# Kernel optimization log

Measured on AMD Instinct MI355X. Metric: run time of the kernel, lower is better.

The kernel has to match this reference:

```python
import jax, jax.numpy as jnp
import numpy as np

N_NODES = 50000
N_EDGES = 1600000
D = 128        # fea_dim == hidden_units == dim_z
L = 3          # num_layers


def _gin_params(key, scale=0.05):
    ks = jax.random.split(key, 7)
    return dict(
        W1=jax.random.normal(ks[0], (L, D, D), jnp.float32) * scale,
        b1=jnp.zeros((L, D), jnp.float32),
        W2=jax.random.normal(ks[1], (L, D, D), jnp.float32) * scale,
        b2=jnp.zeros((L, D), jnp.float32),
        eps=jnp.zeros((L,), jnp.float32),
        Wout=jax.random.normal(ks[2], (D, D), jnp.float32) * scale,
        bout=jnp.zeros((D,), jnp.float32),
    )


def setup_inputs() -> dict:
    key = jax.random.key(0)
    k_x, k_s, k_d, k_m, k_sd = jax.random.split(key, 5)
    inp = {
        'x': jax.random.normal(k_x, (N_NODES, D), jnp.float32),
        'edge_src': jax.random.randint(k_s, (N_EDGES,), 0, N_NODES, jnp.int32),
        'edge_dst': jax.random.randint(k_d, (N_EDGES,), 0, N_NODES, jnp.int32),
    }
    for pref, k in (('mean_', k_m), ('std_', k_sd)):
        for name, v in _gin_params(k).items():
            inp[pref + name] = v
    inp['ln_gamma'] = jnp.ones((D,), jnp.float32)
    inp['ln_beta'] = jnp.zeros((D,), jnp.float32)
    return inp


def _gin(x, src, dst, W1, b1, W2, b2, eps, Wout, bout):
    # Standard GIN: h = MLP((1+eps)*h + sum_{j->i} h_j), Sigmoid activation
    h = x
    n = x.shape[0]
    for l in range(L):
        agg = jax.ops.segment_sum(h[src], dst, num_segments=n)  # [N, D]
        h = (1.0 + eps[l]) * h + agg
        h = jax.nn.sigmoid(h @ W1[l] + b1[l]) @ W2[l] + b2[l]
    return h @ Wout + bout  # [N, dim_z]


def _layernorm(v, g, b, eps=1e-5):
    m = jnp.mean(v, axis=-1, keepdims=True)
    var = jnp.var(v, axis=-1, keepdims=True)
    return (v - m) * jax.lax.rsqrt(var + eps) * g + b


def reference(x, edge_src, edge_dst,
              mean_W1, mean_b1, mean_W2, mean_b2, mean_eps, mean_Wout, mean_bout,
              std_W1, std_b1, std_W2, std_b2, std_eps, std_Wout, std_bout,
              ln_gamma, ln_beta):
    mean_v = _layernorm(_gin(x, edge_src, edge_dst, mean_W1, mean_b1, mean_W2,
                             mean_b2, mean_eps, mean_Wout, mean_bout),
                        ln_gamma, ln_beta)
    # NOTE: source applies bn_mean to the std path too (faithful to bug)
    std_v = _layernorm(_gin(x, edge_src, edge_dst, std_W1, std_b1, std_W2,
                            std_b2, std_eps, std_Wout, std_bout),
                       ln_gamma, ln_beta)
    epsilon = jax.random.normal(jax.random.key(42), mean_v.shape, mean_v.dtype)
    samples = mean_v + epsilon * std_v
    return (samples, mean_v, std_v)
```

## Files before the change

### kernel.cpp

```cpp
#include <hip/hip_runtime.h>
#include <math.h>

#define NNODES 50000
#define NEDGES 1600000
#define DIM    128
#define NHID   (NNODES * DIM)
#define TPB    256
#define NTILES ((NNODES + 63) / 64)

#define NBINS  196
#define BINSZ  256
#define EPT    16
#define CHUNK  (TPB * EPT)
#define NCHUNKS ((NEDGES + CHUNK - 1) / CHUNK)
#define BINCAP 10240

typedef unsigned short bf16_t;
typedef __attribute__((ext_vector_type(8))) short short8;
typedef __attribute__((ext_vector_type(4))) float f32x4;

__device__ __forceinline__ float bf_lo(unsigned u) { return __uint_as_float(u << 16); }
__device__ __forceinline__ float bf_hi(unsigned u) { return __uint_as_float(u & 0xFFFF0000u); }
__device__ __forceinline__ bf16_t f2bf(float f) {
    unsigned u = __float_as_uint(f);
    u += 0x7FFFu + ((u >> 16) & 1u);
    return (bf16_t)(u >> 16);
}
__device__ __forceinline__ unsigned pack2bf(float a, float b) {
    return (unsigned)f2bf(a) | ((unsigned)f2bf(b) << 16);
}

union S8U { short8 v; uint4 u4; unsigned us[4]; };

__global__ __launch_bounds__(TPB) void bin_hist_kernel(
    const int* __restrict__ dst, int* __restrict__ gcnt)
{
    __shared__ int lcnt[NBINS];
    const int tid = threadIdx.x;
    for (int i = tid; i < NBINS; i += TPB) lcnt[i] = 0;
    __syncthreads();
    const int base = blockIdx.x * CHUNK;
    #pragma unroll
    for (int k = 0; k < EPT; ++k) {
        int e = base + k * TPB + tid;
        if (e < NEDGES) atomicAdd(&lcnt[dst[e] >> 8], 1);
    }
    __syncthreads();
    for (int i = tid; i < NBINS; i += TPB) {
        int c = lcnt[i];
        if (c) atomicAdd(&gcnt[i], c);
    }
}

__global__ __launch_bounds__(64) void bin_scan_kernel(
    const int* __restrict__ gcnt, int* __restrict__ start, int* __restrict__ bcur,
    int* __restrict__ off)
{
    const int lane = threadIdx.x;
    int c[4];
    int s = 0;
    #pragma unroll
    for (int k = 0; k < 4; ++k) {
        int b = 4 * lane + k;
        c[k] = (b < NBINS) ? gcnt[b] : 0;
        s += c[k];
    }
    int incl = s;
    #pragma unroll
    for (int d = 1; d < 64; d <<= 1) {
        int t = __shfl_up(incl, d);
        if (lane >= d) incl += t;
    }
    int excl = incl - s;
    #pragma unroll
    for (int k = 0; k < 4; ++k) {
        int b = 4 * lane + k;
        if (b < NBINS) { start[b] = excl; bcur[b] = excl; }
        excl += c[k];
    }
    if (lane == 63) { start[NBINS] = excl; off[NNODES] = excl; }
}

__global__ __launch_bounds__(TPB) void bin_scatter_kernel(
    const int* __restrict__ src, const int* __restrict__ dst,
    int* __restrict__ bcur, unsigned* __restrict__ bucket)
{
    __shared__ int lcnt[NBINS];
    __shared__ int lcur[NBINS];
    const int tid = threadIdx.x;
    for (int i = tid; i < NBINS; i += TPB) lcnt[i] = 0;
    __syncthreads();

    unsigned pk[EPT];
    int bn[EPT];
    const int base = blockIdx.x * CHUNK;
    #pragma unroll
    for (int k = 0; k < EPT; ++k) {
        int e = base + k * TPB + tid;
        int b = -1; unsigned p = 0;
        if (e < NEDGES) {
            int d = dst[e];
            int s = src[e];
            b = d >> 8;
            p = ((unsigned)(d & 255) << 16) | (unsigned)s;
            atomicAdd(&lcnt[b], 1);
        }
        pk[k] = p; bn[k] = b;
    }
    __syncthreads();
    for (int i = tid; i < NBINS; i += TPB) {
        int c = lcnt[i];
        lcur[i] = (c > 0) ? atomicAdd(&bcur[i], c) : 0;
    }
    __syncthreads();
    #pragma unroll
    for (int k = 0; k < EPT; ++k) {
        if (bn[k] >= 0) {
            int p = atomicAdd(&lcur[bn[k]], 1);
            bucket[p] = pk[k];
        }
    }
}

__global__ __launch_bounds__(TPB) void build_csr_kernel(
    const int* __restrict__ start, unsigned* __restrict__ bucket,
    int* __restrict__ off)
{
    __shared__ unsigned se[BINCAP];
    __shared__ int lcnt[BINSZ];
    __shared__ int lofs[BINSZ];
    __shared__ int wsum[4];
    const int tid = threadIdx.x;
    const int b = blockIdx.x;
    const int j0 = start[b], j1 = start[b + 1];
    const int n = j1 - j0;

    lcnt[tid] = 0;
    for (int i = tid; i < n; i += TPB) se[i] = bucket[j0 + i];
    __syncthreads();
    for (int i = tid; i < n; i += TPB) atomicAdd(&lcnt[se[i] >> 16], 1);
    __syncthreads();

    const int lane = tid & 63, wid = tid >> 6;
    int v = lcnt[tid];
    int s = v;
    #pragma unroll
    for (int d = 1; d < 64; d <<= 1) {
        int t = __shfl_up(s, d);
        if (lane >= d) s += t;
    }
    if (lane == 63) wsum[wid] = s;
    __syncthreads();
    if (tid == 0) {
        int a = 0;
        #pragma unroll
        for (int k = 0; k < 4; ++k) { int t = wsum[k]; wsum[k] = a; a += t; }
    }
    __syncthreads();
    int excl = wsum[wid] + s - v;
    lofs[tid] = excl;
    int node = b * BINSZ + tid;
    if (node < NNODES) off[node] = j0 + excl;
    __syncthreads();

    for (int i = tid; i < n; i += TPB) {
        unsigned e = se[i];
        int pos = atomicAdd(&lofs[e >> 16], 1);
        bucket[j0 + pos] = e & 0xFFFFu;
    }
}

__global__ __launch_bounds__(TPB) void gather_agg_f32_kernel(
    const float* __restrict__ h, const int* __restrict__ off,
    const unsigned* __restrict__ bucket, float* __restrict__ agg)
{
    int node = blockIdx.x * (TPB / 64) + (threadIdx.x >> 6);
    int lane = threadIdx.x & 63;
    if (node >= NNODES) return;
    int j0 = off[node], j1 = off[node + 1];
    const float* base = h + 2 * lane;
    float ax = 0.0f, ay = 0.0f;
    int j = j0;
    for (; j + 8 <= j1; j += 8) {
        unsigned s[8];
        #pragma unroll
        for (int k = 0; k < 8; ++k) s[k] = bucket[j + k];
        float2 v[8];
        #pragma unroll
        for (int k = 0; k < 8; ++k) v[k] = *(const float2*)(base + (size_t)s[k] * DIM);
        #pragma unroll
        for (int k = 0; k < 8; ++k) { ax += v[k].x; ay += v[k].y; }
    }
    for (; j < j1; ++j) {
        float2 v0 = *(const float2*)(base + (size_t)bucket[j] * DIM);
        ax += v0.x; ay += v0.y;
    }
    *(float2*)(agg + (size_t)node * DIM + 2 * lane) = make_float2(ax, ay);
}

__global__ __launch_bounds__(TPB) void gather_agg_bf16_kernel(
    const bf16_t* __restrict__ hb, const int* __restrict__ off,
    const unsigned* __restrict__ bucket, float* __restrict__ agg)
{
    int node = blockIdx.x * (TPB / 64) + (threadIdx.x >> 6);
    int lane = threadIdx.x & 63;
    if (node >= NNODES) return;
    int j0 = off[node], j1 = off[node + 1];
    const unsigned* base = (const unsigned*)hb + lane;
    float ax = 0.0f, ay = 0.0f;
    int j = j0;
    for (; j + 8 <= j1; j += 8) {
        unsigned s[8];
        #pragma unroll
        for (int k = 0; k < 8; ++k) s[k] = bucket[j + k];
        unsigned u[8];
        #pragma unroll
        for (int k = 0; k < 8; ++k) u[k] = base[(size_t)s[k] * (DIM / 2)];
        #pragma unroll
        for (int k = 0; k < 8; ++k) { ax += bf_lo(u[k]); ay += bf_hi(u[k]); }
    }
    for (; j < j1; ++j) {
        unsigned u0 = base[(size_t)bucket[j] * (DIM / 2)];
        ax += bf_lo(u0); ay += bf_hi(u0);
    }
    *(float2*)(agg + (size_t)node * DIM + 2 * lane) = make_float2(ax, ay);
}

template <class HinT>
__global__ __launch_bounds__(TPB, 2) void fused_layer_kernel(
    const HinT* __restrict__ hin, const float* __restrict__ agg,
    const float* __restrict__ eps_ptr, int eps_idx,
    const float* __restrict__ W1, const float* __restrict__ b1,
    const float* __restrict__ W2, const float* __restrict__ b2,
    bf16_t* __restrict__ out)
{
    __shared__ short sW1t[128 * 136];
    __shared__ short sW2t[128 * 136];
    float* y1buf = (float*)sW1t;

    const int tid = threadIdx.x;
    #pragma unroll
    for (int it = 0; it < 8; ++it) {
        int idx = it * 256 + tid;
        int n = idx & 127, koct = idx >> 7;
        float f1[8], f2[8];
        #pragma unroll
        for (int j = 0; j < 8; ++j) {
            f1[j] = W1[(8 * koct + j) * 128 + n];
            f2[j] = W2[(8 * koct + j) * 128 + n];
        }
        uint4 u1, u2;
        u1.x = pack2bf(f1[0], f1[1]); u1.y = pack2bf(f1[2], f1[3]);
        u1.z = pack2bf(f1[4], f1[5]); u1.w = pack2bf(f1[6], f1[7]);
        u2.x = pack2bf(f2[0], f2[1]); u2.y = pack2bf(f2[2], f2[3]);
        u2.z = pack2bf(f2[4], f2[5]); u2.w = pack2bf(f2[6], f2[7]);
        *(uint4*)&sW1t[n * 136 + 8 * koct] = u1;
        *(uint4*)&sW2t[n * 136 + 8 * koct] = u2;
    }
    __syncthreads();

    const int lane = tid & 63, w = tid >> 6;
    const int m = lane & 15, quad = lane >> 4;

    short8 bf1[32];
    #pragma unroll
    for (int c = 0; c < 8; ++c)
        #pragma unroll
        for (int k0 = 0; k0 < 4; ++k0)
            bf1[c * 4 + k0] = *(const short8*)&sW1t[(16 * c + m) * 136 + 32 * k0 + 8 * quad];
    __syncthreads();

    const float scale = 1.0f + eps_ptr[eps_idx];
    float b1v[8], b2v[8];
    #pragma unroll
    for (int c = 0; c < 8; ++c) { b1v[c] = b1[16 * c + m]; b2v[c] = b2[16 * c + m]; }

    const int t = blockIdx.x;
    const int arow = min(t * 64 + 16 * w + m, NNODES - 1);
    const size_t rbase = (size_t)arow * DIM;

    short8 afh[4], afl[4];
    #pragma unroll
    for (int k0 = 0; k0 < 4; ++k0) {
        const int kb = 32 * k0 + 8 * quad;
        float zf[8];
        if constexpr (sizeof(HinT) == 4) {
            float4 h0 = *(const float4*)((const float*)hin + rbase + kb);
            float4 h1 = *(const float4*)((const float*)hin + rbase + kb + 4);
            zf[0] = h0.x; zf[1] = h0.y; zf[2] = h0.z; zf[3] = h0.w;
            zf[4] = h1.x; zf[5] = h1.y; zf[6] = h1.z; zf[7] = h1.w;
        } else {
            uint4 hu = *(const uint4*)((const bf16_t*)hin + rbase + kb);
            zf[0] = bf_lo(hu.x); zf[1] = bf_hi(hu.x);
            zf[2] = bf_lo(hu.y); zf[3] = bf_hi(hu.y);
            zf[4] = bf_lo(hu.z); zf[5] = bf_hi(hu.z);
            zf[6] = bf_lo(hu.w); zf[7] = bf_hi(hu.w);
        }
        float4 a0 = *(const float4*)(agg + rbase + kb);
        float4 a1 = *(const float4*)(agg + rbase + kb + 4);
        zf[0] = fmaf(scale, zf[0], a0.x); zf[1] = fmaf(scale, zf[1], a0.y);
        zf[2] = fmaf(scale, zf[2], a0.z); zf[3] = fmaf(scale, zf[3], a0.w);
        zf[4] = fmaf(scale, zf[4], a1.x); zf[5] = fmaf(scale, zf[5], a1.y);
        zf[6] = fmaf(scale, zf[6], a1.z); zf[7] = fmaf(scale, zf[7], a1.w);
        S8U hi;
        hi.us[0] = pack2bf(zf[0], zf[1]); hi.us[1] = pack2bf(zf[2], zf[3]);
        hi.us[2] = pack2bf(zf[4], zf[5]); hi.us[3] = pack2bf(zf[6], zf[7]);
        afh[k0] = hi.v;
        S8U lo;
        float lw[8];
        lw[0] = zf[0] - bf_lo(hi.us[0]); lw[1] = zf[1] - bf_hi(hi.us[0]);
        lw[2] = zf[2] - bf_lo(hi.us[1]); lw[3] = zf[3] - bf_hi(hi.us[1]);
        lw[4] = zf[4] - bf_lo(hi.us[2]); lw[5] = zf[5] - bf_hi(hi.us[2]);
        lw[6] = zf[6] - bf_lo(hi.us[3]); lw[7] = zf[7] - bf_hi(hi.us[3]);
        lo.us[0] = pack2bf(lw[0], lw[1]); lo.us[1] = pack2bf(lw[2], lw[3]);
        lo.us[2] = pack2bf(lw[4], lw[5]); lo.us[3] = pack2bf(lw[6], lw[7]);
        afl[k0] = lo.v;
    }

    f32x4 acc[8];
    #pragma unroll
    for (int c = 0; c < 8; ++c) acc[c] = (f32x4){0.f, 0.f, 0.f, 0.f};
    #pragma unroll
    for (int k0 = 0; k0 < 4; ++k0) {
        #pragma unroll
        for (int c = 0; c < 8; ++c)
            acc[c] = __builtin_amdgcn_mfma_f32_16x16x32_bf16(
                afl[k0], bf1[c * 4 + k0], acc[c], 0, 0, 0);
        #pragma unroll
        for (int c = 0; c < 8; ++c)
            acc[c] = __builtin_amdgcn_mfma_f32_16x16x32_bf16(
                afh[k0], bf1[c * 4 + k0], acc[c], 0, 0, 0);
    }

    const int rloc0 = 16 * w + 4 * quad;
    #pragma unroll
    for (int r = 0; r < 4; ++r) {
        #pragma unroll
        for (int c = 0; c < 8; ++c) {
            float y = acc[c][r] + b1v[c];
            y = 1.0f / (1.0f + expf(-y));
            y1buf[(rloc0 + r) * 132 + 16 * c + m] = y;
        }
    }
    __syncthreads();

    f32x4 acc2[8];
    #pragma unroll
    for (int c = 0; c < 8; ++c) acc2[c] = (f32x4){0.f, 0.f, 0.f, 0.f};
    #pragma unroll
    for (int k0 = 0; k0 < 4; ++k0) {
        const int kb = 32 * k0 + 8 * quad;
        const float* yp = &y1buf[(16 * w + m) * 132 + kb];
        float4 p0 = *(const float4*)yp;
        float4 p1 = *(const float4*)(yp + 4);
        S8U a2;
        a2.us[0] = pack2bf(p0.x, p0.y); a2.us[1] = pack2bf(p0.z, p0.w);
        a2.us[2] = pack2bf(p1.x, p1.y); a2.us[3] = pack2bf(p1.z, p1.w);
        #pragma unroll
        for (int c = 0; c < 8; ++c) {
            short8 b2f = *(const short8*)&sW2t[(16 * c + m) * 136 + kb];
            acc2[c] = __builtin_amdgcn_mfma_f32_16x16x32_bf16(
                a2.v, b2f, acc2[c], 0, 0, 0);
        }
    }

    const int row0 = t * 64 + 16 * w + 4 * quad;
    #pragma unroll
    for (int r = 0; r < 4; ++r) {
        const int grow = row0 + r;
        if (grow < NNODES) {
            bf16_t* op = out + (size_t)grow * DIM + m;
            #pragma unroll
            for (int c = 0; c < 8; ++c) op[16 * c] = f2bf(acc2[c][r] + b2v[c]);
        }
    }
}

template <class HinT, class HoutT, int MODE, bool HAS_AGG, bool SPLIT>
__global__ __launch_bounds__(TPB) void mfma_gemm_kernel(
    const HinT* __restrict__ hin, const float* __restrict__ agg,
    const float* __restrict__ eps_ptr, int eps_idx,
    const float* __restrict__ W, const float* __restrict__ bias,
    const float* __restrict__ gamma, const float* __restrict__ beta,
    HoutT* __restrict__ out)
{
    __shared__ short sWt[128 * 136];

    const int tid = threadIdx.x;
    #pragma unroll
    for (int it = 0; it < 8; ++it) {
        int idx = it * 256 + tid;
        int n = idx & 127, koct = idx >> 7;
        float f[8];
        #pragma unroll
        for (int j = 0; j < 8; ++j) f[j] = W[(8 * koct + j) * 128 + n];
        uint4 u;
        u.x = pack2bf(f[0], f[1]); u.y = pack2bf(f[2], f[3]);
        u.z = pack2bf(f[4], f[5]); u.w = pack2bf(f[6], f[7]);
        *(uint4*)&sWt[n * 136 + 8 * koct] = u;
    }
    __syncthreads();

    const int lane = tid & 63, w = tid >> 6;
    const int m = lane & 15, quad = lane >> 4;

    short8 bf[32];
    #pragma unroll
    for (int c = 0; c < 8; ++c)
        #pragma unroll
        for (int k0 = 0; k0 < 4; ++k0)
            bf[c * 4 + k0] = *(const short8*)&sWt[(16 * c + m) * 136 + 32 * k0 + 8 * quad];

    const float scale = HAS_AGG ? (1.0f + eps_ptr[eps_idx]) : 1.0f;

    float bias_v[8];
    #pragma unroll
    for (int c = 0; c < 8; ++c) bias_v[c] = bias[16 * c + m];
    float g_v[8], bt_v[8];
    if (MODE == 2) {
        #pragma unroll
        for (int c = 0; c < 8; ++c) { g_v[c] = gamma[16 * c + m]; bt_v[c] = beta[16 * c + m]; }
    }

    for (int t = blockIdx.x; t < NTILES; t += gridDim.x) {
        const int arow = min(t * 64 + 16 * w + m, NNODES - 1);
        const size_t rbase = (size_t)arow * DIM;

        short8 afh[4], afl[4];
        #pragma unroll
        for (int k0 = 0; k0 < 4; ++k0) {
            const int kb = 32 * k0 + 8 * quad;
            if (!HAS_AGG && sizeof(HinT) == 2) {
                afh[k0] = *(const short8*)((const bf16_t*)hin + rbase + kb);
            } else {
                float zf[8];
                if constexpr (sizeof(HinT) == 4) {
                    float4 h0 = *(const float4*)((const float*)hin + rbase + kb);
                    float4 h1 = *(const float4*)((const float*)hin + rbase + kb + 4);
                    zf[0] = h0.x; zf[1] = h0.y; zf[2] = h0.z; zf[3] = h0.w;
                    zf[4] = h1.x; zf[5] = h1.y; zf[6] = h1.z; zf[7] = h1.w;
                } else {
                    uint4 hu = *(const uint4*)((const bf16_t*)hin + rbase + kb);
                    zf[0] = bf_lo(hu.x); zf[1] = bf_hi(hu.x);
                    zf[2] = bf_lo(hu.y); zf[3] = bf_hi(hu.y);
                    zf[4] = bf_lo(hu.z); zf[5] = bf_hi(hu.z);
                    zf[6] = bf_lo(hu.w); zf[7] = bf_hi(hu.w);
                }
                if (HAS_AGG) {
                    float4 a0 = *(const float4*)(agg + rbase + kb);
                    float4 a1 = *(const float4*)(agg + rbase + kb + 4);
                    zf[0] = fmaf(scale, zf[0], a0.x); zf[1] = fmaf(scale, zf[1], a0.y);
                    zf[2] = fmaf(scale, zf[2], a0.z); zf[3] = fmaf(scale, zf[3], a0.w);
                    zf[4] = fmaf(scale, zf[4], a1.x); zf[5] = fmaf(scale, zf[5], a1.y);
                    zf[6] = fmaf(scale, zf[6], a1.z); zf[7] = fmaf(scale, zf[7], a1.w);
                }
                S8U hi;
                hi.us[0] = pack2bf(zf[0], zf[1]); hi.us[1] = pack2bf(zf[2], zf[3]);
                hi.us[2] = pack2bf(zf[4], zf[5]); hi.us[3] = pack2bf(zf[6], zf[7]);
                afh[k0] = hi.v;
                if (SPLIT) {
                    S8U lo;
                    float lw[8];
                    lw[0] = zf[0] - bf_lo(hi.us[0]); lw[1] = zf[1] - bf_hi(hi.us[0]);
                    lw[2] = zf[2] - bf_lo(hi.us[1]); lw[3] = zf[3] - bf_hi(hi.us[1]);
                    lw[4] = zf[4] - bf_lo(hi.us[2]); lw[5] = zf[5] - bf_hi(hi.us[2]);
                    lw[6] = zf[6] - bf_lo(hi.us[3]); lw[7] = zf[7] - bf_hi(hi.us[3]);
                    lo.us[0] = pack2bf(lw[0], lw[1]); lo.us[1] = pack2bf(lw[2], lw[3]);
                    lo.us[2] = pack2bf(lw[4], lw[5]); lo.us[3] = pack2bf(lw[6], lw[7]);
                    afl[k0] = lo.v;
                }
            }
        }

        f32x4 acc[8];
        #pragma unroll
        for (int c = 0; c < 8; ++c) acc[c] = (f32x4){0.f, 0.f, 0.f, 0.f};
        #pragma unroll
        for (int k0 = 0; k0 < 4; ++k0) {
            if (SPLIT) {
                #pragma unroll
                for (int c = 0; c < 8; ++c)
                    acc[c] = __builtin_amdgcn_mfma_f32_16x16x32_bf16(
                        afl[k0], bf[c * 4 + k0], acc[c], 0, 0, 0);
            }
            #pragma unroll
            for (int c = 0; c < 8; ++c)
                acc[c] = __builtin_amdgcn_mfma_f32_16x16x32_bf16(
                    afh[k0], bf[c * 4 + k0], acc[c], 0, 0, 0);
        }

        const int row0 = t * 64 + 16 * w + 4 * quad;
        #pragma unroll
        for (int r = 0; r < 4; ++r) {
            const int grow = row0 + r;
            const bool ok = grow < NNODES;
            float y[8];
            #pragma unroll
            for (int c = 0; c < 8; ++c) y[c] = acc[c][r] + bias_v[c];
            if (MODE == 1) {
                #pragma unroll
                for (int c = 0; c < 8; ++c) y[c] = 1.0f / (1.0f + expf(-y[c]));
            } else if (MODE == 2) {
                float s1 = 0.f, s2 = 0.f;
                #pragma unroll
                for (int c = 0; c < 8; ++c) { s1 += y[c]; s2 = fmaf(y[c], y[c], s2); }
                #pragma unroll
                for (int d = 1; d < 16; d <<= 1) {
                    s1 += __shfl_xor(s1, d);
                    s2 += __shfl_xor(s2, d);
                }
                float mean = s1 * (1.0f / DIM);
                float var  = s2 * (1.0f / DIM) - mean * mean;
                float rstd = rsqrtf(var + 1e-5f);
                #pragma unroll
                for (int c = 0; c < 8; ++c)
                    y[c] = fmaf((y[c] - mean) * rstd, g_v[c], bt_v[c]);
            }
            if (ok) {
                if constexpr (sizeof(HoutT) == 4) {
                    float* op = (float*)out + (size_t)grow * DIM + m;
                    #pragma unroll
                    for (int c = 0; c < 8; ++c) op[16 * c] = y[c];
                } else {
                    bf16_t* op = (bf16_t*)out + (size_t)grow * DIM + m;
                    #pragma unroll
                    for (int c = 0; c < 8; ++c) op[16 * c] = f2bf(y[c]);
                }
            }
        }
    }
}

__device__ __forceinline__ unsigned rotl32(unsigned x, int r) {
    return (x << r) | (x >> (32 - r));
}

__device__ __forceinline__ unsigned threefry_xor(unsigned c0, unsigned c1) {
    const unsigned k0 = 0u, k1 = 42u;
    const unsigned k2 = k0 ^ k1 ^ 0x1BD11BDAu;
    unsigned x0 = c0 + k0;
    unsigned x1 = c1 + k1;
#define TF_ROUND(R) { x0 += x1; x1 = rotl32(x1, R); x1 ^= x0; }
    TF_ROUND(13) TF_ROUND(15) TF_ROUND(26) TF_ROUND(6)
    x0 += k1; x1 += k2 + 1u;
    TF_ROUND(17) TF_ROUND(29) TF_ROUND(16) TF_ROUND(24)
    x0 += k2; x1 += k0 + 2u;
    TF_ROUND(13) TF_ROUND(15) TF_ROUND(26) TF_ROUND(6)
    x0 += k0; x1 += k1 + 3u;
    TF_ROUND(17) TF_ROUND(29) TF_ROUND(16) TF_ROUND(24)
    x0 += k1; x1 += k2 + 4u;
    TF_ROUND(13) TF_ROUND(15) TF_ROUND(26) TF_ROUND(6)
    x0 += k2; x1 += k0 + 5u;
#undef TF_ROUND
    return x0 ^ x1;
}

__device__ __forceinline__ float bits_to_normal(unsigned bits) {
    float f = __uint_as_float((bits >> 9) | 0x3F800000u) - 1.0f;
    const float lo = -0.99999994f;
    float u = __fadd_rn(__fmul_rn(f, 2.0f), lo);
    u = fmaxf(lo, u);
    float w = -log1pf(-(u * u));
    float p;
    if (w < 5.0f) {
        w -= 2.5f;
        p = 2.81022636e-08f;
        p = fmaf(p, w, 3.43273939e-07f);
        p = fmaf(p, w, -3.5233877e-06f);
        p = fmaf(p, w, -4.39150654e-06f);
        p = fmaf(p, w, 0.00021858087f);
        p = fmaf(p, w, -0.00125372503f);
        p = fmaf(p, w, -0.00417768164f);
        p = fmaf(p, w, 0.246640727f);
        p = fmaf(p, w, 1.50140941f);
    } else {
        w = sqrtf(w) - 3.0f;
        p = -0.000200214257f;
        p = fmaf(p, w, 0.000100950558f);
        p = fmaf(p, w, 0.00134934322f);
        p = fmaf(p, w, -0.00367342844f);
        p = fmaf(p, w, 0.00573950773f);
        p = fmaf(p, w, -0.0076224613f);
        p = fmaf(p, w, 0.00943887047f);
        p = fmaf(p, w, 1.00167406f);
        p = fmaf(p, w, 2.83297682f);
    }
    return 1.41421356f * (p * u);
}

__global__ __launch_bounds__(TPB) void samples_kernel(
    const float* __restrict__ mean_v, const float* __restrict__ std_v,
    float* __restrict__ samples)
{
    int t = blockIdx.x * TPB + threadIdx.x;
    if (t >= NHID / 4) return;
    float4 m = ((const float4*)mean_v)[t];
    float4 s = ((const float4*)std_v)[t];
    float e[4];
    #pragma unroll
    for (int q = 0; q < 4; q++) {
        unsigned i = 4u * (unsigned)t + (unsigned)q;
        e[q] = bits_to_normal(threefry_xor(0u, i));
    }
    float4 r;
    r.x = fmaf(e[0], s.x, m.x);
    r.y = fmaf(e[1], s.y, m.y);
    r.z = fmaf(e[2], s.z, m.z);
    r.w = fmaf(e[3], s.w, m.w);
    ((float4*)samples)[t] = r;
}

extern "C" void kernel_launch(void* const* d_in, const int* in_sizes, int n_in,
                              void* d_out, int out_size, void* d_ws, size_t ws_size,
                              hipStream_t stream)
{
    const float* x     = (const float*)d_in[0];
    const int*   esrc  = (const int*)d_in[1];
    const int*   edst  = (const int*)d_in[2];
    const float* prm[2][7];
    for (int p = 0; p < 2; p++)
        for (int i = 0; i < 7; i++)
            prm[p][i] = (const float*)d_in[3 + p * 7 + i];
    const float* gamma = (const float*)d_in[17];
    const float* beta  = (const float*)d_in[18];

    float*  S  = (float*)d_out;
    bf16_t* Sb = (bf16_t*)d_out;
    float*  M  = S + NHID;
    float*  V  = M + NHID;

    int* gcnt  = (int*)d_ws;
    int* start = gcnt + NBINS;
    int* bcur  = start + NBINS + 1;
    int* off   = bcur + NBINS;
    unsigned* bucket = (unsigned*)(off + NNODES + 1);

    const dim3 gChunk(NCHUNKS);
    const dim3 gBin(NBINS);
    const dim3 gGather((NNODES + (TPB / 64) - 1) / (TPB / 64));
    const dim3 gTile(NTILES);
    const dim3 gSamp((NHID / 4 + TPB - 1) / TPB);

    hipMemsetAsync(gcnt, 0, NBINS * sizeof(int), stream);
    bin_hist_kernel<<<gChunk, TPB, 0, stream>>>(edst, gcnt);
    bin_scan_kernel<<<1, 64, 0, stream>>>(gcnt, start, bcur, off);
    bin_scatter_kernel<<<gChunk, TPB, 0, stream>>>(esrc, edst, bcur, bucket);
    build_csr_kernel<<<gBin, TPB, 0, stream>>>(start, bucket, off);

    gather_agg_f32_kernel<<<gGather, TPB, 0, stream>>>(x, off, bucket, V);

    for (int p = 0; p < 2; p++) {
        const float* W1  = prm[p][0];
        const float* b1  = prm[p][1];
        const float* W2  = prm[p][2];
        const float* b2  = prm[p][3];
        const float* eps = prm[p][4];
        const float* Wo  = prm[p][5];
        const float* bo  = prm[p][6];
        float* AGG = (p == 0) ? M : V;
        float* OUT = (p == 0) ? M : V;

        fused_layer_kernel<float><<<gTile, TPB, 0, stream>>>(
            x, V, eps, 0, W1, b1, W2, b2, Sb);

        for (int l = 1; l < 3; l++) {
            gather_agg_bf16_kernel<<<gGather, TPB, 0, stream>>>(Sb, off, bucket, AGG);
            fused_layer_kernel<bf16_t><<<gTile, TPB, 0, stream>>>(
                Sb, AGG, eps, l, W1 + (size_t)l * DIM * DIM, b1 + l * DIM,
                W2 + (size_t)l * DIM * DIM, b2 + l * DIM, Sb);
        }

        mfma_gemm_kernel<bf16_t, float, 2, false, false><<<gTile, TPB, 0, stream>>>(
            Sb, nullptr, nullptr, 0, Wo, bo, gamma, beta, OUT);
    }

    samples_kernel<<<gSamp, TPB, 0, stream>>>(M, V, S);
}
```

Baseline: 713.7 us.

## Batch mean and std GIN paths into concatenated gathers and doubled-grid layer kernels

Both GIN branches (mean and std) are now processed together. Hidden states are stored interleaved as 256-wide bf16 rows, so one gather pass reads both paths' 128-wide halves of each neighbor row and writes a 256-wide float aggregate. Each layer and the final projection launch one kernel with twice as many blocks, and each block picks its path's weights. This halves the number of CSR gather traversals and kernel launches and fetches both paths per edge together. In exchange, gather rows are twice as wide, and the ACAT scratch (N×256 floats) overlaps the M/V output buffers, which the final projection must overwrite in place.

```diff
diff --git a/kernel.cpp b/kernel.cpp
--- a/kernel.cpp
+++ b/kernel.cpp
@@ -172,7 +172,7 @@
 
 __global__ __launch_bounds__(TPB) void gather_agg_f32_kernel(
     const float* __restrict__ h, const int* __restrict__ off,
-    const unsigned* __restrict__ bucket, float* __restrict__ agg)
+    const unsigned* __restrict__ bucket, float* __restrict__ acat)
 {
     int node = blockIdx.x * (TPB / 64) + (threadIdx.x >> 6);
     int lane = threadIdx.x & 63;
@@ -195,48 +195,72 @@
         float2 v0 = *(const float2*)(base + (size_t)bucket[j] * DIM);
         ax += v0.x; ay += v0.y;
     }
-    *(float2*)(agg + (size_t)node * DIM + 2 * lane) = make_float2(ax, ay);
-}
-
-__global__ __launch_bounds__(TPB) void gather_agg_bf16_kernel(
-    const bf16_t* __restrict__ hb, const int* __restrict__ off,
-    const unsigned* __restrict__ bucket, float* __restrict__ agg)
+    *(float2*)(acat + (size_t)node * 256 + 2 * lane) = make_float2(ax, ay);
+}
+
+__global__ __launch_bounds__(TPB) void gather_cat_kernel(
+    const bf16_t* __restrict__ hc, const int* __restrict__ off,
+    const unsigned* __restrict__ bucket, float* __restrict__ acat)
 {
     int node = blockIdx.x * (TPB / 64) + (threadIdx.x >> 6);
     int lane = threadIdx.x & 63;
     if (node >= NNODES) return;
     int j0 = off[node], j1 = off[node + 1];
-    const unsigned* base = (const unsigned*)hb + lane;
-    float ax = 0.0f, ay = 0.0f;
+    const unsigned* base = (const unsigned*)hc;
+    float ax = 0.f, ay = 0.f, bx = 0.f, by = 0.f;
     int j = j0;
     for (; j + 8 <= j1; j += 8) {
         unsigned s[8];
         #pragma unroll
         for (int k = 0; k < 8; ++k) s[k] = bucket[j + k];
-        unsigned u[8];
-        #pragma unroll
-        for (int k = 0; k < 8; ++k) u[k] = base[(size_t)s[k] * (DIM / 2)];
-        #pragma unroll
-        for (int k = 0; k < 8; ++k) { ax += bf_lo(u[k]); ay += bf_hi(u[k]); }
+        unsigned um[8], uv[8];
+        #pragma unroll
+        for (int k = 0; k < 8; ++k) {
+            const unsigned* rp = base + (size_t)s[k] * 128;
+            um[k] = rp[lane];
+            uv[k] = rp[64 + lane];
+        }
+        #pragma unroll
+        for (int k = 0; k < 8; ++k) {
+            ax += bf_lo(um[k]); ay += bf_hi(um[k]);
+            bx += bf_lo(uv[k]); by += bf_hi(uv[k]);
+        }
     }
     for (; j < j1; ++j) {
-        unsigned u0 = base[(size_t)bucket[j] * (DIM / 2)];
-        ax += bf_lo(u0); ay += bf_hi(u0);
-    }
-    *(float2*)(agg + (size_t)node * DIM + 2 * lane) = make_float2(ax, ay);
-}
-
-template <class HinT>
+        const unsigned* rp = base + (size_t)bucket[j] * 128;
+        unsigned um = rp[lane], uv = rp[64 + lane];
+        ax += bf_lo(um); ay += bf_hi(um);
+        bx += bf_lo(uv); by += bf_hi(uv);
+    }
+    float* ar = acat + (size_t)node * 256;
+    *(float2*)(ar + 2 * lane)       = make_float2(ax, ay);
+    *(float2*)(ar + 128 + 2 * lane) = make_float2(bx, by);
+}
+
+template <class HinT, int INSTRIDE>
 __global__ __launch_bounds__(TPB, 2) void fused_layer_kernel(
-    const HinT* __restrict__ hin, const float* __restrict__ agg,
-    const float* __restrict__ eps_ptr, int eps_idx,
-    const float* __restrict__ W1, const float* __restrict__ b1,
-    const float* __restrict__ W2, const float* __restrict__ b2,
+    const HinT* __restrict__ hin, const float* __restrict__ acat, int aggByPath,
+    const float* __restrict__ eps0, const float* __restrict__ eps1, int eps_idx,
+    const float* __restrict__ W1_0, const float* __restrict__ b1_0,
+    const float* __restrict__ W2_0, const float* __restrict__ b2_0,
+    const float* __restrict__ W1_1, const float* __restrict__ b1_1,
+    const float* __restrict__ W2_1, const float* __restrict__ b2_1,
     bf16_t* __restrict__ out)
 {
     __shared__ short sW1t[128 * 136];
     __shared__ short sW2t[128 * 136];
     float* y1buf = (float*)sW1t;
+
+    const int p = (blockIdx.x >= NTILES) ? 1 : 0;
+    const int t = blockIdx.x - p * NTILES;
+    const float* W1 = p ? W1_1 : W1_0;
+    const float* b1 = p ? b1_1 : b1_0;
+    const float* W2 = p ? W2_1 : W2_0;
+    const float* b2 = p ? b2_1 : b2_0;
+    const float* epsp = p ? eps1 : eps0;
+    const HinT* hbase = (INSTRIDE == 256) ? (hin + p * 128) : hin;
+    const float* abase = acat + (aggByPath ? p * 128 : 0);
+    bf16_t* ob = out + p * 128;
 
     const int tid = threadIdx.x;
     #pragma unroll
@@ -270,14 +294,12 @@
             bf1[c * 4 + k0] = *(const short8*)&sW1t[(16 * c + m) * 136 + 32 * k0 + 8 * quad];
     __syncthreads();
 
-    const float scale = 1.0f + eps_ptr[eps_idx];
+    const float scale = 1.0f + epsp[eps_idx];
     float b1v[8], b2v[8];
     #pragma unroll
     for (int c = 0; c < 8; ++c) { b1v[c] = b1[16 * c + m]; b2v[c] = b2[16 * c + m]; }
 
-    const int t = blockIdx.x;
     const int arow = min(t * 64 + 16 * w + m, NNODES - 1);
-    const size_t rbase = (size_t)arow * DIM;
 
     short8 afh[4], afl[4];
     #pragma unroll
@@ -285,19 +307,21 @@
         const int kb = 32 * k0 + 8 * quad;
         float zf[8];
         if constexpr (sizeof(HinT) == 4) {
-            float4 h0 = *(const float4*)((const float*)hin + rbase + kb);
-            float4 h1 = *(const float4*)((const float*)hin + rbase + kb + 4);
+            const float* hp = (const float*)hbase + (size_t)arow * INSTRIDE + kb;
+            float4 h0 = *(const float4*)hp;
+            float4 h1 = *(const float4*)(hp + 4);
             zf[0] = h0.x; zf[1] = h0.y; zf[2] = h0.z; zf[3] = h0.w;
             zf[4] = h1.x; zf[5] = h1.y; zf[6] = h1.z; zf[7] = h1.w;
         } else {
-            uint4 hu = *(const uint4*)((const bf16_t*)hin + rbase + kb);
+            uint4 hu = *(const uint4*)((const bf16_t*)hbase + (size_t)arow * INSTRIDE + kb);
             zf[0] = bf_lo(hu.x); zf[1] = bf_hi(hu.x);
             zf[2] = bf_lo(hu.y); zf[3] = bf_hi(hu.y);
             zf[4] = bf_lo(hu.z); zf[5] = bf_hi(hu.z);
             zf[6] = bf_lo(hu.w); zf[7] = bf_hi(hu.w);
         }
-        float4 a0 = *(const float4*)(agg + rbase + kb);
-        float4 a1 = *(const float4*)(agg + rbase + kb + 4);
+        const float* ap = abase + (size_t)arow * 256 + kb;
+        float4 a0 = *(const float4*)ap;
+        float4 a1 = *(const float4*)(ap + 4);
         zf[0] = fmaf(scale, zf[0], a0.x); zf[1] = fmaf(scale, zf[1], a0.y);
         zf[2] = fmaf(scale, zf[2], a0.z); zf[3] = fmaf(scale, zf[3], a0.w);
         zf[4] = fmaf(scale, zf[4], a1.x); zf[5] = fmaf(scale, zf[5], a1.y);
@@ -369,22 +393,28 @@
     for (int r = 0; r < 4; ++r) {
         const int grow = row0 + r;
         if (grow < NNODES) {
-            bf16_t* op = out + (size_t)grow * DIM + m;
+            bf16_t* op = ob + (size_t)grow * 256 + m;
             #pragma unroll
             for (int c = 0; c < 8; ++c) op[16 * c] = f2bf(acc2[c][r] + b2v[c]);
         }
     }
 }
 
-template <class HinT, class HoutT, int MODE, bool HAS_AGG, bool SPLIT>
-__global__ __launch_bounds__(TPB) void mfma_gemm_kernel(
-    const HinT* __restrict__ hin, const float* __restrict__ agg,
-    const float* __restrict__ eps_ptr, int eps_idx,
-    const float* __restrict__ W, const float* __restrict__ bias,
+__global__ __launch_bounds__(TPB) void final_proj_kernel(
+    const bf16_t* __restrict__ hc,
+    const float* __restrict__ Wo0, const float* __restrict__ bo0,
+    const float* __restrict__ Wo1, const float* __restrict__ bo1,
     const float* __restrict__ gamma, const float* __restrict__ beta,
-    HoutT* __restrict__ out)
+    float* __restrict__ M, float* __restrict__ V)
 {
     __shared__ short sWt[128 * 136];
+
+    const int p = (blockIdx.x >= NTILES) ? 1 : 0;
+    const int t = blockIdx.x - p * NTILES;
+    const float* W = p ? Wo1 : Wo0;
+    const float* bias = p ? bo1 : bo0;
+    const bf16_t* hbase = hc + p * 128;
+    float* out = p ? V : M;
 
     const int tid = threadIdx.x;
     #pragma unroll
@@ -411,122 +441,53 @@
         for (int k0 = 0; k0 < 4; ++k0)
             bf[c * 4 + k0] = *(const short8*)&sWt[(16 * c + m) * 136 + 32 * k0 + 8 * quad];
 
-    const float scale = HAS_AGG ? (1.0f + eps_ptr[eps_idx]) : 1.0f;
-
-    float bias_v[8];
-    #pragma unroll
-    for (int c = 0; c < 8; ++c) bias_v[c] = bias[16 * c + m];
-    float g_v[8], bt_v[8];
-    if (MODE == 2) {
-        #pragma unroll
-        for (int c = 0; c < 8; ++c) { g_v[c] = gamma[16 * c + m]; bt_v[c] = beta[16 * c + m]; }
-    }
-
-    for (int t = blockIdx.x; t < NTILES; t += gridDim.x) {
-        const int arow = min(t * 64 + 16 * w + m, NNODES - 1);
-        const size_t rbase = (size_t)arow * DIM;
-
-        short8 afh[4], afl[4];
-        #pragma unroll
-        for (int k0 = 0; k0 < 4; ++k0) {
-            const int kb = 32 * k0 + 8 * quad;
-            if (!HAS_AGG && sizeof(HinT) == 2) {
-                afh[k0] = *(const short8*)((const bf16_t*)hin + rbase + kb);
-            } else {
-                float zf[8];
-                if constexpr (sizeof(HinT) == 4) {
-                    float4 h0 = *(const float4*)((const float*)hin + rbase + kb);
-                    float4 h1 = *(const float4*)((const float*)hin + rbase + kb + 4);
-                    zf[0] = h0.x; zf[1] = h0.y; zf[2] = h0.z; zf[3] = h0.w;
-                    zf[4] = h1.x; zf[5] = h1.y; zf[6] = h1.z; zf[7] = h1.w;
-                } else {
-                    uint4 hu = *(const uint4*)((const bf16_t*)hin + rbase + kb);
-                    zf[0] = bf_lo(hu.x); zf[1] = bf_hi(hu.x);
-                    zf[2] = bf_lo(hu.y); zf[3] = bf_hi(hu.y);
-                    zf[4] = bf_lo(hu.z); zf[5] = bf_hi(hu.z);
-                    zf[6] = bf_lo(hu.w); zf[7] = bf_hi(hu.w);
-                }
-                if (HAS_AGG) {
-                    float4 a0 = *(const float4*)(agg + rbase + kb);
-                    float4 a1 = *(const float4*)(agg + rbase + kb + 4);
-                    zf[0] = fmaf(scale, zf[0], a0.x); zf[1] = fmaf(scale, zf[1], a0.y);
-                    zf[2] = fmaf(scale, zf[2], a0.z); zf[3] = fmaf(scale, zf[3], a0.w);
-                    zf[4] = fmaf(scale, zf[4], a1.x); zf[5] = fmaf(scale, zf[5], a1.y);
-                    zf[6] = fmaf(scale, zf[6], a1.z); zf[7] = fmaf(scale, zf[7], a1.w);
-                }
-                S8U hi;
-                hi.us[0] = pack2bf(zf[0], zf[1]); hi.us[1] = pack2bf(zf[2], zf[3]);
-                hi.us[2] = pack2bf(zf[4], zf[5]); hi.us[3] = pack2bf(zf[6], zf[7]);
-                afh[k0] = hi.v;
-                if (SPLIT) {
-                    S8U lo;
-                    float lw[8];
-                    lw[0] = zf[0] - bf_lo(hi.us[0]); lw[1] = zf[1] - bf_hi(hi.us[0]);
-                    lw[2] = zf[2] - bf_lo(hi.us[1]); lw[3] = zf[3] - bf_hi(hi.us[1]);
-                    lw[4] = zf[4] - bf_lo(hi.us[2]); lw[5] = zf[5] - bf_hi(hi.us[2]);
-                    lw[6] = zf[6] - bf_lo(hi.us[3]); lw[7] = zf[7] - bf_hi(hi.us[3]);
-                    lo.us[0] = pack2bf(lw[0], lw[1]); lo.us[1] = pack2bf(lw[2], lw[3]);
-                    lo.us[2] = pack2bf(lw[4], lw[5]); lo.us[3] = pack2bf(lw[6], lw[7]);
-                    afl[k0] = lo.v;
-                }
-            }
-        }
-
-        f32x4 acc[8];
-        #pragma unroll
-        for (int c = 0; c < 8; ++c) acc[c] = (f32x4){0.f, 0.f, 0.f, 0.f};
-        #pragma unroll
-        for (int k0 = 0; k0 < 4; ++k0) {
-            if (SPLIT) {
-                #pragma unroll
-                for (int c = 0; c < 8; ++c)
-                    acc[c] = __builtin_amdgcn_mfma_f32_16x16x32_bf16(
-                        afl[k0], bf[c * 4 + k0], acc[c], 0, 0, 0);
-            }
+    float bias_v[8], g_v[8], bt_v[8];
+    #pragma unroll
+    for (int c = 0; c < 8; ++c) {
+        bias_v[c] = bias[16 * c + m];
+        g_v[c] = gamma[16 * c + m];
+        bt_v[c] = beta[16 * c + m];
+    }
+
+    const int arow = min(t * 64 + 16 * w + m, NNODES - 1);
+    short8 af[4];
+    #pragma unroll
+    for (int k0 = 0; k0 < 4; ++k0)
+        af[k0] = *(const short8*)(hbase + (size_t)arow * 256 + 32 * k0 + 8 * quad);
+
+    f32x4 acc[8];
+    #pragma unroll
+    for (int c = 0; c < 8; ++c) acc[c] = (f32x4){0.f, 0.f, 0.f, 0.f};
+    #pragma unroll
+    for (int k0 = 0; k0 < 4; ++k0)
+        #pragma unroll
+        for (int c = 0; c < 8; ++c)
+            acc[c] = __builtin_amdgcn_mfma_f32_16x16x32_bf16(
+                af[k0], bf[c * 4 + k0], acc[c], 0, 0, 0);
+
+    const int row0 = t * 64 + 16 * w + 4 * quad;
+    #pragma unroll
+    for (int r = 0; r < 4; ++r) {
+        const int grow = row0 + r;
+        float y[8];
+        #pragma unroll
+        for (int c = 0; c < 8; ++c) y[c] = acc[c][r] + bias_v[c];
+        float s1 = 0.f, s2 = 0.f;
+        #pragma unroll
+        for (int c = 0; c < 8; ++c) { s1 += y[c]; s2 = fmaf(y[c], y[c], s2); }
+        #pragma unroll
+        for (int d = 1; d < 16; d <<= 1) {
+            s1 += __shfl_xor(s1, d);
+            s2 += __shfl_xor(s2, d);
+        }
+        float mean = s1 * (1.0f / DIM);
+        float var  = s2 * (1.0f / DIM) - mean * mean;
+        float rstd = rsqrtf(var + 1e-5f);
+        if (grow < NNODES) {
+            float* op = out + (size_t)grow * DIM + m;
             #pragma unroll
             for (int c = 0; c < 8; ++c)
-                acc[c] = __builtin_amdgcn_mfma_f32_16x16x32_bf16(
-                    afh[k0], bf[c * 4 + k0], acc[c], 0, 0, 0);
-        }
-
-        const int row0 = t * 64 + 16 * w + 4 * quad;
-        #pragma unroll
-        for (int r = 0; r < 4; ++r) {
-            const int grow = row0 + r;
-            const bool ok = grow < NNODES;
-            float y[8];
-            #pragma unroll
-            for (int c = 0; c < 8; ++c) y[c] = acc[c][r] + bias_v[c];
-            if (MODE == 1) {
-                #pragma unroll
-                for (int c = 0; c < 8; ++c) y[c] = 1.0f / (1.0f + expf(-y[c]));
-            } else if (MODE == 2) {
-                float s1 = 0.f, s2 = 0.f;
-                #pragma unroll
-                for (int c = 0; c < 8; ++c) { s1 += y[c]; s2 = fmaf(y[c], y[c], s2); }
-                #pragma unroll
-                for (int d = 1; d < 16; d <<= 1) {
-                    s1 += __shfl_xor(s1, d);
-                    s2 += __shfl_xor(s2, d);
-                }
-                float mean = s1 * (1.0f / DIM);
-                float var  = s2 * (1.0f / DIM) - mean * mean;
-                float rstd = rsqrtf(var + 1e-5f);
-                #pragma unroll
-                for (int c = 0; c < 8; ++c)
-                    y[c] = fmaf((y[c] - mean) * rstd, g_v[c], bt_v[c]);
-            }
-            if (ok) {
-                if constexpr (sizeof(HoutT) == 4) {
-                    float* op = (float*)out + (size_t)grow * DIM + m;
-                    #pragma unroll
-                    for (int c = 0; c < 8; ++c) op[16 * c] = y[c];
-                } else {
-                    bf16_t* op = (bf16_t*)out + (size_t)grow * DIM + m;
-                    #pragma unroll
-                    for (int c = 0; c < 8; ++c) op[16 * c] = f2bf(y[c]);
-                }
-            }
+                op[16 * c] = fmaf((y[c] - mean) * rstd, g_v[c], bt_v[c]);
         }
     }
 }
@@ -625,9 +586,10 @@
     const float* beta  = (const float*)d_in[18];
 
     float*  S  = (float*)d_out;
-    bf16_t* Sb = (bf16_t*)d_out;
     float*  M  = S + NHID;
     float*  V  = M + NHID;
+    bf16_t* Hc = (bf16_t*)S;
+    float*  ACAT = M;
 
     int* gcnt  = (int*)d_ws;
     int* start = gcnt + NBINS;
@@ -638,7 +600,7 @@
     const dim3 gChunk(NCHUNKS);
     const dim3 gBin(NBINS);
     const dim3 gGather((NNODES + (TPB / 64) - 1) / (TPB / 64));
-    const dim3 gTile(NTILES);
+    const dim3 gTile2(2 * NTILES);
     const dim3 gSamp((NHID / 4 + TPB - 1) / TPB);
 
     hipMemsetAsync(gcnt, 0, NBINS * sizeof(int), stream);
@@ -647,32 +609,25 @@
     bin_scatter_kernel<<<gChunk, TPB, 0, stream>>>(esrc, edst, bcur, bucket);
     build_csr_kernel<<<gBin, TPB, 0, stream>>>(start, bucket, off);
 
-    gather_agg_f32_kernel<<<gGather, TPB, 0, stream>>>(x, off, bucket, V);
-
-    for (int p = 0; p < 2; p++) {
-        const float* W1  = prm[p][0];
-        const float* b1  = prm[p][1];
-        const float* W2  = prm[p][2];
-        const float* b2  = prm[p][3];
-        const float* eps = prm[p][4];
-        const float* Wo  = prm[p][5];
-        const float* bo  = prm[p][6];
-        float* AGG = (p == 0) ? M : V;
-        float* OUT = (p == 0) ? M : V;
-
-        fused_layer_kernel<float><<<gTile, TPB, 0, stream>>>(
-            x, V, eps, 0, W1, b1, W2, b2, Sb);
-
-        for (int l = 1; l < 3; l++) {
-            gather_agg_bf16_kernel<<<gGather, TPB, 0, stream>>>(Sb, off, bucket, AGG);
-            fused_layer_kernel<bf16_t><<<gTile, TPB, 0, stream>>>(
-                Sb, AGG, eps, l, W1 + (size_t)l * DIM * DIM, b1 + l * DIM,
-                W2 + (size_t)l * DIM * DIM, b2 + l * DIM, Sb);
-        }
-
-        mfma_gemm_kernel<bf16_t, float, 2, false, false><<<gTile, TPB, 0, stream>>>(
-            Sb, nullptr, nullptr, 0, Wo, bo, gamma, beta, OUT);
-    }
+    gather_agg_f32_kernel<<<gGather, TPB, 0, stream>>>(x, off, bucket, ACAT);
+
+    fused_layer_kernel<float, DIM><<<gTile2, TPB, 0, stream>>>(
+        x, ACAT, 0, prm[0][4], prm[1][4], 0,
+        prm[0][0], prm[0][1], prm[0][2], prm[0][3],
+        prm[1][0], prm[1][1], prm[1][2], prm[1][3], Hc);
+
+    for (int l = 1; l < 3; l++) {
+        gather_cat_kernel<<<gGather, TPB, 0, stream>>>(Hc, off, bucket, ACAT);
+        fused_layer_kernel<bf16_t, 256><<<gTile2, TPB, 0, stream>>>(
+            Hc, ACAT, 1, prm[0][4], prm[1][4], l,
+            prm[0][0] + (size_t)l * DIM * DIM, prm[0][1] + l * DIM,
+            prm[0][2] + (size_t)l * DIM * DIM, prm[0][3] + l * DIM,
+            prm[1][0] + (size_t)l * DIM * DIM, prm[1][1] + l * DIM,
+            prm[1][2] + (size_t)l * DIM * DIM, prm[1][3] + l * DIM, Hc);
+    }
+
+    final_proj_kernel<<<gTile2, TPB, 0, stream>>>(
+        Hc, prm[0][5], prm[0][6], prm[1][5], prm[1][6], gamma, beta, M, V);
 
     samples_kernel<<<gSamp, TPB, 0, stream>>>(M, V, S);
 }
```

New measurement: 671.3 us. 5.9% less time.
